# Kernel optimization log

Hardware: AMD Instinct MI355X
Metric: run time of the kernel (lower is better)

Reference implementation:

```python
import jax, jax.numpy as jnp
import numpy as np

B, H, L, D = 2, 16, 2048, 64

def setup_inputs() -> dict:
    key = jax.random.key(0)
    kq, kk, kv, km = jax.random.split(key, 4)
    q = jax.random.normal(kq, (B, H, L, D), dtype=jnp.float32)
    k = jax.random.normal(kk, (B, H, L, D), dtype=jnp.float32)
    v = jax.random.normal(kv, (B, H, L, D), dtype=jnp.float32)
    mask = jax.random.randint(km, (B, 1, L, L), 0, 2, dtype=jnp.int32)
    return {"q": q, "k": k, "v": v, "mask": mask}

def reference(q, k, v, mask):
    d_tensor = q.shape[-1]
    # score: [B,H,L,L] = q @ k^T / sqrt(d)
    score = jnp.einsum("bhqd,bhkd->bhqk", q, k) / jnp.sqrt(jnp.float32(d_tensor))
    score = jnp.where(mask == 0, jnp.float32(-jnp.inf), score)
    score = jax.nn.softmax(score, axis=-1)
    # torch.nan_to_num(nan=0.0): rows fully masked produce NaN -> 0
    score = jnp.where(jnp.isnan(score), jnp.float32(0.0), score)
    # dropout=0.0 (eval / p=0) -> identity
    out = jnp.einsum("bhqk,bhkd->bhqd", score, v)
    return (out, score)
```

## Files before the change

### kernel.cpp

```cpp
#include <hip/hip_runtime.h>
#include <math.h>

#define B_ 2
#define H_ 16
#define L_ 2048
#define D_ 64
#define NCH (L_ / 64)
#define NWG (B_ * H_ * (L_ / 64))
#define OUT_ELEMS ((size_t)B_ * H_ * L_ * D_)
#define WPR (L_ / 16)
#define C1 0.180336880f

typedef _Float16 half8 __attribute__((ext_vector_type(8)));
typedef _Float16 half4_t __attribute__((ext_vector_type(4)));
typedef float f32x4 __attribute__((ext_vector_type(4)));
typedef int i32x4 __attribute__((ext_vector_type(4)));
typedef unsigned int u32;
typedef unsigned short u16;
typedef u16 u16x4 __attribute__((ext_vector_type(4)));
typedef u32 u32x4 __attribute__((ext_vector_type(4)));
typedef u32 u32x2 __attribute__((ext_vector_type(2)));

#define SWZ(row, colh) ((colh) ^ (((row) & 7) << 3))

__global__ __launch_bounds__(256) void pack_kernel(
    const int* __restrict__ M, u16* __restrict__ pmask)
{
  const int idx = blockIdx.x * 256 + threadIdx.x;
  const int* src = M + (size_t)idx * 16;
  u32 w = 0;
#pragma unroll
  for (int j = 0; j < 4; ++j) {
    i32x4 m = ((const i32x4*)src)[j];
#pragma unroll
    for (int r = 0; r < 4; ++r)
      w |= (m[r] != 0 ? 1u : 0u) << (j * 4 + r);
  }
  pmask[idx] = (u16)w;
}

__global__ __launch_bounds__(256, 4) void lsum_kernel(
    const float* __restrict__ Q, const float* __restrict__ K,
    const u16* __restrict__ pmask, float* __restrict__ lpart)
{
  const int qt = blockIdx.x, h = blockIdx.y;
  const int b = blockIdx.z >> 2, kq = blockIdx.z & 3;
  const int bh = b * H_ + h;
  const int q0 = qt * 64, k0 = kq * 512;
  const int tid = threadIdx.x;
  const int wv = tid >> 6, lane = tid & 63;
  const int lr = lane & 15, lg = lane >> 4;
  const int qrow = q0 + wv * 16 + lr;

  __shared__ _Float16 Kbuf[2][64 * 64];

  const float* kbase = K + (size_t)bh * L_ * D_ + (size_t)k0 * D_;
  const u16* pmrow = pmask + (size_t)(b * L_ + qrow) * WPR + (k0 >> 4);

  half8 qf[2];
  {
    const float* qr = Q + (size_t)(bh * L_ + qrow) * D_;
#pragma unroll
    for (int f = 0; f < 2; ++f) {
      f32x4 x = *(const f32x4*)(qr + f * 32 + lg * 8);
      f32x4 y = *(const f32x4*)(qr + f * 32 + lg * 8 + 4);
      qf[f] = half8{(_Float16)(x[0]*C1), (_Float16)(x[1]*C1), (_Float16)(x[2]*C1), (_Float16)(x[3]*C1),
                    (_Float16)(y[0]*C1), (_Float16)(y[1]*C1), (_Float16)(y[2]*C1), (_Float16)(y[3]*C1)};
    }
  }

  const int ksr = tid >> 2, ksd = (tid & 3) * 16;
  auto loadK4 = [&](int kc, f32x4* r) {
    const float* s = kbase + (size_t)(kc + ksr) * D_ + ksd;
    r[0] = ((const f32x4*)s)[0]; r[1] = ((const f32x4*)s)[1];
    r[2] = ((const f32x4*)s)[2]; r[3] = ((const f32x4*)s)[3];
  };
  auto writeK = [&](int buf, const f32x4* r) {
    half8 lo = half8{(_Float16)r[0][0], (_Float16)r[0][1], (_Float16)r[0][2], (_Float16)r[0][3],
                     (_Float16)r[1][0], (_Float16)r[1][1], (_Float16)r[1][2], (_Float16)r[1][3]};
    half8 hi = half8{(_Float16)r[2][0], (_Float16)r[2][1], (_Float16)r[2][2], (_Float16)r[2][3],
                     (_Float16)r[3][0], (_Float16)r[3][1], (_Float16)r[3][2], (_Float16)r[3][3]};
    *(half8*)&Kbuf[buf][(ksr << 6) + SWZ(ksr, ksd)] = lo;
    *(half8*)&Kbuf[buf][(ksr << 6) + SWZ(ksr, ksd + 8)] = hi;
  };

  float l_l = 0.f;
  {
    f32x4 kr[4];
    loadK4(0, kr);
    writeK(0, kr);
  }
  __syncthreads();

  for (int c = 0; c < 8; ++c) {
    const int kc = c * 64, cur = c & 1;
    f32x4 kr[4];
    if (c < 7) loadK4(kc + 64, kr);
    u16x4 pm = *(const u16x4*)(pmrow + c * 4);

    f32x4 acc[4] = {f32x4{0,0,0,0}, f32x4{0,0,0,0}, f32x4{0,0,0,0}, f32x4{0,0,0,0}};
    __builtin_amdgcn_s_setprio(1);
#pragma unroll
    for (int kb = 0; kb < 4; ++kb) {
      int row = kb * 16 + lr;
      half8 a0 = *(const half8*)&Kbuf[cur][(row << 6) + SWZ(row, lg * 8)];
      half8 a1 = *(const half8*)&Kbuf[cur][(row << 6) + SWZ(row, 32 + lg * 8)];
      acc[kb] = __builtin_amdgcn_mfma_f32_16x16x32_f16(a0, qf[0], acc[kb], 0, 0, 0);
      acc[kb] = __builtin_amdgcn_mfma_f32_16x16x32_f16(a1, qf[1], acc[kb], 0, 0, 0);
    }
    __builtin_amdgcn_s_setprio(0);

    float cs = 0.f;
#pragma unroll
    for (int kb = 0; kb < 4; ++kb)
#pragma unroll
      for (int r = 0; r < 4; ++r)
        cs += exp2f(((pm[kb] >> (lg * 4 + r)) & 1) ? acc[kb][r] : -INFINITY);
    l_l += cs;

    if (c < 7) writeK(cur ^ 1, kr);
    __syncthreads();
  }

  l_l += __shfl_xor(l_l, 16);
  l_l += __shfl_xor(l_l, 32);
  if (lg == 0)
    lpart[((size_t)kq * 32 + bh) * L_ + qrow] = l_l;
}

__global__ __launch_bounds__(256, 4) void attn_kernel(
    const float* __restrict__ Q, const float* __restrict__ K,
    const float* __restrict__ V, const u16* __restrict__ pmask,
    const float* __restrict__ lpart,
    float* __restrict__ out, float* __restrict__ score)
{
  const int bid = blockIdx.x;
  const int lid = (bid & 7) * (NWG / 8) + (bid >> 3);
  const int qt = lid & 31, h = (lid >> 5) & 15, b = lid >> 9;

  const int bh = b * H_ + h;
  const int q0 = qt * 64;
  const int tid = threadIdx.x;
  const int wv = tid >> 6, lane = tid & 63;
  const int lr = lane & 15, lg = lane >> 4;
  const int qrow = q0 + wv * 16 + lr;

  __shared__ _Float16 Klds[2][64 * 64];
  __shared__ _Float16 Vlds[2][64 * 64];

  const float* kbase = K + (size_t)bh * L_ * D_;
  const float* vbase = V + (size_t)bh * L_ * D_;
  const u16* pmrow = pmask + (size_t)(b * L_ + qrow) * WPR;
  float* srow = score + ((size_t)bh * L_ + qrow) * L_;
  float* ob = out + (size_t)(bh * L_ + q0) * D_;

  float lsum = 0.f;
#pragma unroll
  for (int kq = 0; kq < 4; ++kq)
    lsum += lpart[((size_t)kq * 32 + bh) * L_ + qrow];
  const float inv_l = (lsum > 0.f) ? 1.f / lsum : 0.f;

  half8 qf[2];
  {
    const float* qr = Q + (size_t)(bh * L_ + qrow) * D_;
#pragma unroll
    for (int f = 0; f < 2; ++f) {
      f32x4 x = *(const f32x4*)(qr + f * 32 + lg * 8);
      f32x4 y = *(const f32x4*)(qr + f * 32 + lg * 8 + 4);
      qf[f] = half8{(_Float16)(x[0]*C1), (_Float16)(x[1]*C1), (_Float16)(x[2]*C1), (_Float16)(x[3]*C1),
                    (_Float16)(y[0]*C1), (_Float16)(y[1]*C1), (_Float16)(y[2]*C1), (_Float16)(y[3]*C1)};
    }
  }

  const int ksr = tid >> 2, ksd = (tid & 3) * 16;
  const int vk0 = (tid & 15) * 4, vd0 = (tid >> 4) * 4;

  auto loadK4 = [&](int kc, f32x4* r) {
    const float* s = kbase + (size_t)(kc + ksr) * D_ + ksd;
    r[0] = ((const f32x4*)s)[0]; r[1] = ((const f32x4*)s)[1];
    r[2] = ((const f32x4*)s)[2]; r[3] = ((const f32x4*)s)[3];
  };
  auto writeK = [&](int buf, const f32x4* r) {
    half8 lo = half8{(_Float16)r[0][0], (_Float16)r[0][1], (_Float16)r[0][2], (_Float16)r[0][3],
                     (_Float16)r[1][0], (_Float16)r[1][1], (_Float16)r[1][2], (_Float16)r[1][3]};
    half8 hi = half8{(_Float16)r[2][0], (_Float16)r[2][1], (_Float16)r[2][2], (_Float16)r[2][3],
                     (_Float16)r[3][0], (_Float16)r[3][1], (_Float16)r[3][2], (_Float16)r[3][3]};
    *(half8*)&Klds[buf][(ksr << 6) + SWZ(ksr, ksd)] = lo;
    *(half8*)&Klds[buf][(ksr << 6) + SWZ(ksr, ksd + 8)] = hi;
  };
  auto loadV4 = [&](int kc, f32x4* r) {
#pragma unroll
    for (int i = 0; i < 4; ++i)
      r[i] = *(const f32x4*)(vbase + (size_t)(kc + vk0 + i) * D_ + vd0);
  };
  auto writeV = [&](int buf, const f32x4* r) {
#pragma unroll
    for (int j = 0; j < 4; ++j) {
      int row = vd0 + j;
      *(half4_t*)&Vlds[buf][(row << 6) + SWZ(row, vk0)] =
          half4_t{(_Float16)r[0][j], (_Float16)r[1][j],
                  (_Float16)r[2][j], (_Float16)r[3][j]};
    }
  };

  {
    f32x4 kr[4], vr[4];
    loadK4(0, kr);
    loadV4(0, vr);
    writeK(0, kr);
    writeV(0, vr);
  }
  __syncthreads();

  f32x4 o_acc[4] = {f32x4{0,0,0,0}, f32x4{0,0,0,0}, f32x4{0,0,0,0}, f32x4{0,0,0,0}};

  const int s0lane = lr + 32 * (lg & 1);
  const int s1lane = s0lane + 16;
  const bool hisel = (lg & 2) != 0;

  for (int c = 0; c < NCH; ++c) {
    const int kc = c * 64, cur = c & 1;
    f32x4 krP[4], vrP[4];
    if (c < NCH - 1) {
      loadK4(kc + 64, krP);
      loadV4(kc + 64, vrP);
    }
    u16x4 pm = *(const u16x4*)(pmrow + c * 4);

    f32x4 acc[4] = {f32x4{0,0,0,0}, f32x4{0,0,0,0}, f32x4{0,0,0,0}, f32x4{0,0,0,0}};
    __builtin_amdgcn_s_setprio(1);
#pragma unroll
    for (int kb = 0; kb < 4; ++kb) {
      int row = kb * 16 + lr;
      half8 a0 = *(const half8*)&Klds[cur][(row << 6) + SWZ(row, lg * 8)];
      half8 a1 = *(const half8*)&Klds[cur][(row << 6) + SWZ(row, 32 + lg * 8)];
      acc[kb] = __builtin_amdgcn_mfma_f32_16x16x32_f16(a0, qf[0], acc[kb], 0, 0, 0);
      acc[kb] = __builtin_amdgcn_mfma_f32_16x16x32_f16(a1, qf[1], acc[kb], 0, 0, 0);
    }
    __builtin_amdgcn_s_setprio(0);

    u32 phu[8];
#pragma unroll
    for (int kb = 0; kb < 4; ++kb) {
      f32x4 p4;
#pragma unroll
      for (int r = 0; r < 4; ++r)
        p4[r] = exp2f(((pm[kb] >> (lg * 4 + r)) & 1) ? acc[kb][r] : -INFINITY) * inv_l;
      __builtin_nontemporal_store(p4, (f32x4*)(srow + kc + kb * 16 + lg * 4));
      half4_t hp = half4_t{(_Float16)p4[0], (_Float16)p4[1],
                           (_Float16)p4[2], (_Float16)p4[3]};
      u32x2 uu = __builtin_bit_cast(u32x2, hp);
      phu[2 * kb] = uu[0];
      phu[2 * kb + 1] = uu[1];
    }

    __builtin_amdgcn_s_setprio(1);
#pragma unroll
    for (int ks = 0; ks < 2; ++ks) {
      int a0 = __shfl((int)phu[4 * ks + 0], s0lane);
      int a1 = __shfl((int)phu[4 * ks + 1], s0lane);
      int a2 = __shfl((int)phu[4 * ks + 2], s0lane);
      int a3 = __shfl((int)phu[4 * ks + 3], s0lane);
      int b0 = __shfl((int)phu[4 * ks + 0], s1lane);
      int b1 = __shfl((int)phu[4 * ks + 1], s1lane);
      int b2 = __shfl((int)phu[4 * ks + 2], s1lane);
      int b3 = __shfl((int)phu[4 * ks + 3], s1lane);
      u32x4 pau = u32x4{(u32)(hisel ? a2 : a0), (u32)(hisel ? a3 : a1),
                        (u32)(hisel ? b2 : b0), (u32)(hisel ? b3 : b1)};
      half8 pa = __builtin_bit_cast(half8, pau);
#pragma unroll
      for (int db = 0; db < 4; ++db) {
        int row = db * 16 + lr;
        half8 vf = *(const half8*)&Vlds[cur][(row << 6) + SWZ(row, ks * 32 + lg * 8)];
        o_acc[db] = __builtin_amdgcn_mfma_f32_16x16x32_f16(pa, vf, o_acc[db], 0, 0, 0);
      }
    }
    __builtin_amdgcn_s_setprio(0);

    if (c < NCH - 1) {
      writeK(cur ^ 1, krP);
      writeV(cur ^ 1, vrP);
    }
    __syncthreads();
  }

#pragma unroll
  for (int db = 0; db < 4; ++db)
#pragma unroll
    for (int r = 0; r < 4; ++r)
      __builtin_nontemporal_store(
          o_acc[db][r], ob + (size_t)(wv * 16 + lg * 4 + r) * D_ + db * 16 + lr);
}

extern "C" void kernel_launch(void* const* d_in, const int* in_sizes, int n_in,
                              void* d_out, int out_size, void* d_ws, size_t ws_size,
                              hipStream_t stream) {
  const float* q = (const float*)d_in[0];
  const float* k = (const float*)d_in[1];
  const float* v = (const float*)d_in[2];
  const int* mask = (const int*)d_in[3];
  float* out = (float*)d_out;
  float* score = out + OUT_ELEMS;

  u16* pmask = (u16*)d_ws;
  float* lpart = (float*)((char*)d_ws + (1 << 20));

  pack_kernel<<<dim3(B_ * L_ * WPR / 256), 256, 0, stream>>>(mask, pmask);
  lsum_kernel<<<dim3(32, 16, 8), 256, 0, stream>>>(q, k, pmask, lpart);
  attn_kernel<<<dim3(NWG), 256, 0, stream>>>(q, k, v, pmask, lpart, out, score);
}
```

Baseline: 247.2 us.

## Split attention into split-K PV pass with atomics, separate score pass, and rescale

The row-sum pass is merged with the unnormalized P·V product, split four ways along keys, and each split adds its partial output into a zeroed buffer with atomics. A separate kernel then writes the normalized score matrix over two key halves, and a final kernel divides the output by the row sums. The aim is more workgroups and shorter serial loops than the old single 32-chunk attention kernel, and moving the large score write out of the MFMA loop. The cost is a memset, extra kernel launches, float atomics whose ordering can vary, QK^T computed twice, and P·V accumulated from unnormalized fp16 probabilities, which risks precision loss.

```diff
diff --git a/kernel.cpp b/kernel.cpp
--- a/kernel.cpp
+++ b/kernel.cpp
@@ -5,8 +5,6 @@
 #define H_ 16
 #define L_ 2048
 #define D_ 64
-#define NCH (L_ / 64)
-#define NWG (B_ * H_ * (L_ / 64))
 #define OUT_ELEMS ((size_t)B_ * H_ * L_ * D_)
 #define WPR (L_ / 16)
 #define C1 0.180336880f
@@ -39,12 +37,14 @@
   pmask[idx] = (u16)w;
 }
 
-__global__ __launch_bounds__(256, 4) void lsum_kernel(
+__global__ __launch_bounds__(256, 4) void lsum_pv_kernel(
     const float* __restrict__ Q, const float* __restrict__ K,
-    const u16* __restrict__ pmask, float* __restrict__ lpart)
+    const float* __restrict__ V, const u16* __restrict__ pmask,
+    float* __restrict__ lpart, float* __restrict__ out)
 {
-  const int qt = blockIdx.x, h = blockIdx.y;
-  const int b = blockIdx.z >> 2, kq = blockIdx.z & 3;
+  const int bid = blockIdx.x;
+  const int lid = (bid & 7) * (4096 / 8) + (bid >> 3);
+  const int qt = lid & 31, kq = (lid >> 5) & 3, h = (lid >> 7) & 15, b = lid >> 11;
   const int bh = b * H_ + h;
   const int q0 = qt * 64, k0 = kq * 512;
   const int tid = threadIdx.x;
@@ -52,113 +52,13 @@
   const int lr = lane & 15, lg = lane >> 4;
   const int qrow = q0 + wv * 16 + lr;
 
-  __shared__ _Float16 Kbuf[2][64 * 64];
-
-  const float* kbase = K + (size_t)bh * L_ * D_ + (size_t)k0 * D_;
-  const u16* pmrow = pmask + (size_t)(b * L_ + qrow) * WPR + (k0 >> 4);
-
-  half8 qf[2];
-  {
-    const float* qr = Q + (size_t)(bh * L_ + qrow) * D_;
-#pragma unroll
-    for (int f = 0; f < 2; ++f) {
-      f32x4 x = *(const f32x4*)(qr + f * 32 + lg * 8);
-      f32x4 y = *(const f32x4*)(qr + f * 32 + lg * 8 + 4);
-      qf[f] = half8{(_Float16)(x[0]*C1), (_Float16)(x[1]*C1), (_Float16)(x[2]*C1), (_Float16)(x[3]*C1),
-                    (_Float16)(y[0]*C1), (_Float16)(y[1]*C1), (_Float16)(y[2]*C1), (_Float16)(y[3]*C1)};
-    }
-  }
-
-  const int ksr = tid >> 2, ksd = (tid & 3) * 16;
-  auto loadK4 = [&](int kc, f32x4* r) {
-    const float* s = kbase + (size_t)(kc + ksr) * D_ + ksd;
-    r[0] = ((const f32x4*)s)[0]; r[1] = ((const f32x4*)s)[1];
-    r[2] = ((const f32x4*)s)[2]; r[3] = ((const f32x4*)s)[3];
-  };
-  auto writeK = [&](int buf, const f32x4* r) {
-    half8 lo = half8{(_Float16)r[0][0], (_Float16)r[0][1], (_Float16)r[0][2], (_Float16)r[0][3],
-                     (_Float16)r[1][0], (_Float16)r[1][1], (_Float16)r[1][2], (_Float16)r[1][3]};
-    half8 hi = half8{(_Float16)r[2][0], (_Float16)r[2][1], (_Float16)r[2][2], (_Float16)r[2][3],
-                     (_Float16)r[3][0], (_Float16)r[3][1], (_Float16)r[3][2], (_Float16)r[3][3]};
-    *(half8*)&Kbuf[buf][(ksr << 6) + SWZ(ksr, ksd)] = lo;
-    *(half8*)&Kbuf[buf][(ksr << 6) + SWZ(ksr, ksd + 8)] = hi;
-  };
-
-  float l_l = 0.f;
-  {
-    f32x4 kr[4];
-    loadK4(0, kr);
-    writeK(0, kr);
-  }
-  __syncthreads();
-
-  for (int c = 0; c < 8; ++c) {
-    const int kc = c * 64, cur = c & 1;
-    f32x4 kr[4];
-    if (c < 7) loadK4(kc + 64, kr);
-    u16x4 pm = *(const u16x4*)(pmrow + c * 4);
-
-    f32x4 acc[4] = {f32x4{0,0,0,0}, f32x4{0,0,0,0}, f32x4{0,0,0,0}, f32x4{0,0,0,0}};
-    __builtin_amdgcn_s_setprio(1);
-#pragma unroll
-    for (int kb = 0; kb < 4; ++kb) {
-      int row = kb * 16 + lr;
-      half8 a0 = *(const half8*)&Kbuf[cur][(row << 6) + SWZ(row, lg * 8)];
-      half8 a1 = *(const half8*)&Kbuf[cur][(row << 6) + SWZ(row, 32 + lg * 8)];
-      acc[kb] = __builtin_amdgcn_mfma_f32_16x16x32_f16(a0, qf[0], acc[kb], 0, 0, 0);
-      acc[kb] = __builtin_amdgcn_mfma_f32_16x16x32_f16(a1, qf[1], acc[kb], 0, 0, 0);
-    }
-    __builtin_amdgcn_s_setprio(0);
-
-    float cs = 0.f;
-#pragma unroll
-    for (int kb = 0; kb < 4; ++kb)
-#pragma unroll
-      for (int r = 0; r < 4; ++r)
-        cs += exp2f(((pm[kb] >> (lg * 4 + r)) & 1) ? acc[kb][r] : -INFINITY);
-    l_l += cs;
-
-    if (c < 7) writeK(cur ^ 1, kr);
-    __syncthreads();
-  }
-
-  l_l += __shfl_xor(l_l, 16);
-  l_l += __shfl_xor(l_l, 32);
-  if (lg == 0)
-    lpart[((size_t)kq * 32 + bh) * L_ + qrow] = l_l;
-}
-
-__global__ __launch_bounds__(256, 4) void attn_kernel(
-    const float* __restrict__ Q, const float* __restrict__ K,
-    const float* __restrict__ V, const u16* __restrict__ pmask,
-    const float* __restrict__ lpart,
-    float* __restrict__ out, float* __restrict__ score)
-{
-  const int bid = blockIdx.x;
-  const int lid = (bid & 7) * (NWG / 8) + (bid >> 3);
-  const int qt = lid & 31, h = (lid >> 5) & 15, b = lid >> 9;
-
-  const int bh = b * H_ + h;
-  const int q0 = qt * 64;
-  const int tid = threadIdx.x;
-  const int wv = tid >> 6, lane = tid & 63;
-  const int lr = lane & 15, lg = lane >> 4;
-  const int qrow = q0 + wv * 16 + lr;
-
   __shared__ _Float16 Klds[2][64 * 64];
   __shared__ _Float16 Vlds[2][64 * 64];
 
-  const float* kbase = K + (size_t)bh * L_ * D_;
-  const float* vbase = V + (size_t)bh * L_ * D_;
-  const u16* pmrow = pmask + (size_t)(b * L_ + qrow) * WPR;
-  float* srow = score + ((size_t)bh * L_ + qrow) * L_;
+  const float* kbase = K + ((size_t)bh * L_ + k0) * D_;
+  const float* vbase = V + ((size_t)bh * L_ + k0) * D_;
+  const u16* pmrow = pmask + (size_t)(b * L_ + qrow) * WPR + (k0 >> 4);
   float* ob = out + (size_t)(bh * L_ + q0) * D_;
-
-  float lsum = 0.f;
-#pragma unroll
-  for (int kq = 0; kq < 4; ++kq)
-    lsum += lpart[((size_t)kq * 32 + bh) * L_ + qrow];
-  const float inv_l = (lsum > 0.f) ? 1.f / lsum : 0.f;
 
   half8 qf[2];
   {
@@ -205,26 +105,22 @@
 
   {
     f32x4 kr[4], vr[4];
-    loadK4(0, kr);
-    loadV4(0, vr);
-    writeK(0, kr);
-    writeV(0, vr);
+    loadK4(0, kr); loadV4(0, vr);
+    writeK(0, kr); writeV(0, vr);
   }
   __syncthreads();
 
+  float l_l = 0.f;
   f32x4 o_acc[4] = {f32x4{0,0,0,0}, f32x4{0,0,0,0}, f32x4{0,0,0,0}, f32x4{0,0,0,0}};
 
   const int s0lane = lr + 32 * (lg & 1);
   const int s1lane = s0lane + 16;
   const bool hisel = (lg & 2) != 0;
 
-  for (int c = 0; c < NCH; ++c) {
+  for (int c = 0; c < 8; ++c) {
     const int kc = c * 64, cur = c & 1;
     f32x4 krP[4], vrP[4];
-    if (c < NCH - 1) {
-      loadK4(kc + 64, krP);
-      loadV4(kc + 64, vrP);
-    }
+    if (c < 7) { loadK4(kc + 64, krP); loadV4(kc + 64, vrP); }
     u16x4 pm = *(const u16x4*)(pmrow + c * 4);
 
     f32x4 acc[4] = {f32x4{0,0,0,0}, f32x4{0,0,0,0}, f32x4{0,0,0,0}, f32x4{0,0,0,0}};
@@ -244,9 +140,10 @@
     for (int kb = 0; kb < 4; ++kb) {
       f32x4 p4;
 #pragma unroll
-      for (int r = 0; r < 4; ++r)
-        p4[r] = exp2f(((pm[kb] >> (lg * 4 + r)) & 1) ? acc[kb][r] : -INFINITY) * inv_l;
-      __builtin_nontemporal_store(p4, (f32x4*)(srow + kc + kb * 16 + lg * 4));
+      for (int r = 0; r < 4; ++r) {
+        p4[r] = exp2f(((pm[kb] >> (lg * 4 + r)) & 1) ? acc[kb][r] : -INFINITY);
+        l_l += p4[r];
+      }
       half4_t hp = half4_t{(_Float16)p4[0], (_Float16)p4[1],
                            (_Float16)p4[2], (_Float16)p4[3]};
       u32x2 uu = __builtin_bit_cast(u32x2, hp);
@@ -277,19 +174,130 @@
     }
     __builtin_amdgcn_s_setprio(0);
 
-    if (c < NCH - 1) {
-      writeK(cur ^ 1, krP);
-      writeV(cur ^ 1, vrP);
-    }
+    if (c < 7) { writeK(cur ^ 1, krP); writeV(cur ^ 1, vrP); }
     __syncthreads();
   }
 
+  l_l += __shfl_xor(l_l, 16);
+  l_l += __shfl_xor(l_l, 32);
+  if (lg == 0)
+    lpart[((size_t)kq * 32 + bh) * L_ + qrow] = l_l;
+
 #pragma unroll
   for (int db = 0; db < 4; ++db)
 #pragma unroll
     for (int r = 0; r < 4; ++r)
-      __builtin_nontemporal_store(
-          o_acc[db][r], ob + (size_t)(wv * 16 + lg * 4 + r) * D_ + db * 16 + lr);
+      atomicAdd(&ob[(size_t)(wv * 16 + lg * 4 + r) * D_ + db * 16 + lr],
+                o_acc[db][r]);
+}
+
+__global__ __launch_bounds__(256, 8) void score_kernel(
+    const float* __restrict__ Q, const float* __restrict__ K,
+    const u16* __restrict__ pmask, const float* __restrict__ lpart,
+    float* __restrict__ score)
+{
+  const int bid = blockIdx.x;
+  const int lid = (bid & 7) * (2048 / 8) + (bid >> 3);
+  const int qt = lid & 31, kh = (lid >> 5) & 1, h = (lid >> 6) & 15, b = lid >> 10;
+  const int bh = b * H_ + h;
+  const int q0 = qt * 64, k0 = kh * 1024;
+  const int tid = threadIdx.x;
+  const int wv = tid >> 6, lane = tid & 63;
+  const int lr = lane & 15, lg = lane >> 4;
+  const int qrow = q0 + wv * 16 + lr;
+
+  __shared__ _Float16 Kbuf[2][64 * 64];
+
+  const float* kbase = K + ((size_t)bh * L_ + k0) * D_;
+  const u16* pmrow = pmask + (size_t)(b * L_ + qrow) * WPR + (k0 >> 4);
+  float* srow = score + ((size_t)bh * L_ + qrow) * L_ + k0;
+
+  float lsum = 0.f;
+#pragma unroll
+  for (int kq = 0; kq < 4; ++kq)
+    lsum += lpart[((size_t)kq * 32 + bh) * L_ + qrow];
+  const float inv_l = (lsum > 0.f) ? 1.f / lsum : 0.f;
+
+  half8 qf[2];
+  {
+    const float* qr = Q + (size_t)(bh * L_ + qrow) * D_;
+#pragma unroll
+    for (int f = 0; f < 2; ++f) {
+      f32x4 x = *(const f32x4*)(qr + f * 32 + lg * 8);
+      f32x4 y = *(const f32x4*)(qr + f * 32 + lg * 8 + 4);
+      qf[f] = half8{(_Float16)(x[0]*C1), (_Float16)(x[1]*C1), (_Float16)(x[2]*C1), (_Float16)(x[3]*C1),
+                    (_Float16)(y[0]*C1), (_Float16)(y[1]*C1), (_Float16)(y[2]*C1), (_Float16)(y[3]*C1)};
+    }
+  }
+
+  const int ksr = tid >> 2, ksd = (tid & 3) * 16;
+  auto loadK4 = [&](int kc, f32x4* r) {
+    const float* s = kbase + (size_t)(kc + ksr) * D_ + ksd;
+    r[0] = ((const f32x4*)s)[0]; r[1] = ((const f32x4*)s)[1];
+    r[2] = ((const f32x4*)s)[2]; r[3] = ((const f32x4*)s)[3];
+  };
+  auto writeK = [&](int buf, const f32x4* r) {
+    half8 lo = half8{(_Float16)r[0][0], (_Float16)r[0][1], (_Float16)r[0][2], (_Float16)r[0][3],
+                     (_Float16)r[1][0], (_Float16)r[1][1], (_Float16)r[1][2], (_Float16)r[1][3]};
+    half8 hi = half8{(_Float16)r[2][0], (_Float16)r[2][1], (_Float16)r[2][2], (_Float16)r[2][3],
+                     (_Float16)r[3][0], (_Float16)r[3][1], (_Float16)r[3][2], (_Float16)r[3][3]};
+    *(half8*)&Kbuf[buf][(ksr << 6) + SWZ(ksr, ksd)] = lo;
+    *(half8*)&Kbuf[buf][(ksr << 6) + SWZ(ksr, ksd + 8)] = hi;
+  };
+
+  {
+    f32x4 kr[4];
+    loadK4(0, kr);
+    writeK(0, kr);
+  }
+  __syncthreads();
+
+  for (int c = 0; c < 16; ++c) {
+    const int kc = c * 64, cur = c & 1;
+    f32x4 kr[4];
+    if (c < 15) loadK4(kc + 64, kr);
+    u16x4 pm = *(const u16x4*)(pmrow + c * 4);
+
+    f32x4 acc[4] = {f32x4{0,0,0,0}, f32x4{0,0,0,0}, f32x4{0,0,0,0}, f32x4{0,0,0,0}};
+    __builtin_amdgcn_s_setprio(1);
+#pragma unroll
+    for (int kb = 0; kb < 4; ++kb) {
+      int row = kb * 16 + lr;
+      half8 a0 = *(const half8*)&Kbuf[cur][(row << 6) + SWZ(row, lg * 8)];
+      half8 a1 = *(const half8*)&Kbuf[cur][(row << 6) + SWZ(row, 32 + lg * 8)];
+      acc[kb] = __builtin_amdgcn_mfma_f32_16x16x32_f16(a0, qf[0], acc[kb], 0, 0, 0);
+      acc[kb] = __builtin_amdgcn_mfma_f32_16x16x32_f16(a1, qf[1], acc[kb], 0, 0, 0);
+    }
+    __builtin_amdgcn_s_setprio(0);
+
+#pragma unroll
+    for (int kb = 0; kb < 4; ++kb) {
+      f32x4 p4;
+#pragma unroll
+      for (int r = 0; r < 4; ++r)
+        p4[r] = exp2f(((pm[kb] >> (lg * 4 + r)) & 1) ? acc[kb][r] : -INFINITY) * inv_l;
+      __builtin_nontemporal_store(p4, (f32x4*)(srow + kc + kb * 16 + lg * 4));
+    }
+
+    if (c < 15) writeK(cur ^ 1, kr);
+    __syncthreads();
+  }
+}
+
+__global__ __launch_bounds__(256) void scale_kernel(
+    const float* __restrict__ lpart, float* __restrict__ out)
+{
+  const int idx = blockIdx.x * 256 + threadIdx.x;
+  const int row = idx >> 4;
+  const int bh = row >> 11, qrow = row & (L_ - 1);
+  float ls = lpart[(size_t)(0 * 32 + bh) * L_ + qrow]
+           + lpart[(size_t)(1 * 32 + bh) * L_ + qrow]
+           + lpart[(size_t)(2 * 32 + bh) * L_ + qrow]
+           + lpart[(size_t)(3 * 32 + bh) * L_ + qrow];
+  const float inv = (ls > 0.f) ? 1.f / ls : 0.f;
+  f32x4 v = ((const f32x4*)out)[idx];
+  v[0] *= inv; v[1] *= inv; v[2] *= inv; v[3] *= inv;
+  __builtin_nontemporal_store(v, (f32x4*)out + idx);
 }
 
 extern "C" void kernel_launch(void* const* d_in, const int* in_sizes, int n_in,
@@ -305,7 +313,9 @@
   u16* pmask = (u16*)d_ws;
   float* lpart = (float*)((char*)d_ws + (1 << 20));
 
+  hipMemsetAsync(out, 0, OUT_ELEMS * sizeof(float), stream);
   pack_kernel<<<dim3(B_ * L_ * WPR / 256), 256, 0, stream>>>(mask, pmask);
-  lsum_kernel<<<dim3(32, 16, 8), 256, 0, stream>>>(q, k, pmask, lpart);
-  attn_kernel<<<dim3(NWG), 256, 0, stream>>>(q, k, v, pmask, lpart, out, score);
-}
+  lsum_pv_kernel<<<dim3(4096), 256, 0, stream>>>(q, k, v, pmask, lpart, out);
+  score_kernel<<<dim3(2048), 256, 0, stream>>>(q, k, pmask, lpart, score);
+  scale_kernel<<<dim3(OUT_ELEMS / 4 / 256), 256, 0, stream>>>(lpart, out);
+}
```

After: 345.7 us. 1.4x slower.

## Split attention key range across two workgroups and combine partial outputs

Applied to the files above, without the earlier changes.

Splits the attention kernel's key dimension in two, so each workgroup handles half of the keys. This doubles the grid from 1024 to 2048 blocks and gives the GPU more parallelism and better latency hiding. Each half writes its partial output to its own buffer, and a new combine kernel adds the halves. Because the softmax normalizer is precomputed globally, the partial sums can simply be added. This costs an extra kernel launch plus an extra write and read of the output-sized buffer, and it falls back to the full kernel if the workspace is too small.

```diff
diff --git a/kernel.cpp b/kernel.cpp
--- a/kernel.cpp
+++ b/kernel.cpp
@@ -5,8 +5,6 @@
 #define H_ 16
 #define L_ 2048
 #define D_ 64
-#define NCH (L_ / 64)
-#define NWG (B_ * H_ * (L_ / 64))
 #define OUT_ELEMS ((size_t)B_ * H_ * L_ * D_)
 #define WPR (L_ / 16)
 #define C1 0.180336880f
@@ -54,7 +52,7 @@
 
   __shared__ _Float16 Kbuf[2][64 * 64];
 
-  const float* kbase = K + (size_t)bh * L_ * D_ + (size_t)k0 * D_;
+  const float* kbase = K + ((size_t)bh * L_ + k0) * D_;
   const u16* pmrow = pmask + (size_t)(b * L_ + qrow) * WPR + (k0 >> 4);
 
   half8 qf[2];
@@ -128,16 +126,12 @@
     lpart[((size_t)kq * 32 + bh) * L_ + qrow] = l_l;
 }
 
-__global__ __launch_bounds__(256, 4) void attn_kernel(
-    const float* __restrict__ Q, const float* __restrict__ K,
-    const float* __restrict__ V, const u16* __restrict__ pmask,
-    const float* __restrict__ lpart,
-    float* __restrict__ out, float* __restrict__ score)
-{
-  const int bid = blockIdx.x;
-  const int lid = (bid & 7) * (NWG / 8) + (bid >> 3);
-  const int qt = lid & 31, h = (lid >> 5) & 15, b = lid >> 9;
-
+template <int KCH>
+__device__ __forceinline__ void attn_body(
+    const float* Q, const float* K, const float* V,
+    const u16* pmask, const float* lpart,
+    float* obase, float* score, int b, int h, int qt, int k0)
+{
   const int bh = b * H_ + h;
   const int q0 = qt * 64;
   const int tid = threadIdx.x;
@@ -148,11 +142,11 @@
   __shared__ _Float16 Klds[2][64 * 64];
   __shared__ _Float16 Vlds[2][64 * 64];
 
-  const float* kbase = K + (size_t)bh * L_ * D_;
-  const float* vbase = V + (size_t)bh * L_ * D_;
-  const u16* pmrow = pmask + (size_t)(b * L_ + qrow) * WPR;
-  float* srow = score + ((size_t)bh * L_ + qrow) * L_;
-  float* ob = out + (size_t)(bh * L_ + q0) * D_;
+  const float* kbase = K + ((size_t)bh * L_ + k0) * D_;
+  const float* vbase = V + ((size_t)bh * L_ + k0) * D_;
+  const u16* pmrow = pmask + (size_t)(b * L_ + qrow) * WPR + (k0 >> 4);
+  float* srow = score + ((size_t)bh * L_ + qrow) * L_ + k0;
+  float* ob = obase + (size_t)(bh * L_ + q0) * D_;
 
   float lsum = 0.f;
 #pragma unroll
@@ -205,10 +199,8 @@
 
   {
     f32x4 kr[4], vr[4];
-    loadK4(0, kr);
-    loadV4(0, vr);
-    writeK(0, kr);
-    writeV(0, vr);
+    loadK4(0, kr); loadV4(0, vr);
+    writeK(0, kr); writeV(0, vr);
   }
   __syncthreads();
 
@@ -218,10 +210,10 @@
   const int s1lane = s0lane + 16;
   const bool hisel = (lg & 2) != 0;
 
-  for (int c = 0; c < NCH; ++c) {
+  for (int c = 0; c < KCH; ++c) {
     const int kc = c * 64, cur = c & 1;
     f32x4 krP[4], vrP[4];
-    if (c < NCH - 1) {
+    if (c < KCH - 1) {
       loadK4(kc + 64, krP);
       loadV4(kc + 64, vrP);
     }
@@ -277,7 +269,7 @@
     }
     __builtin_amdgcn_s_setprio(0);
 
-    if (c < NCH - 1) {
+    if (c < KCH - 1) {
       writeK(cur ^ 1, krP);
       writeV(cur ^ 1, vrP);
     }
@@ -288,8 +280,42 @@
   for (int db = 0; db < 4; ++db)
 #pragma unroll
     for (int r = 0; r < 4; ++r)
-      __builtin_nontemporal_store(
-          o_acc[db][r], ob + (size_t)(wv * 16 + lg * 4 + r) * D_ + db * 16 + lr);
+      ob[(size_t)(wv * 16 + lg * 4 + r) * D_ + db * 16 + lr] = o_acc[db][r];
+}
+
+__global__ __launch_bounds__(256, 4) void attn_split_kernel(
+    const float* __restrict__ Q, const float* __restrict__ K,
+    const float* __restrict__ V, const u16* __restrict__ pmask,
+    const float* __restrict__ lpart,
+    float* __restrict__ op0, float* __restrict__ op1, float* __restrict__ score)
+{
+  const int bid = blockIdx.x;
+  const int lid = (bid & 7) * (2048 / 8) + (bid >> 3);
+  const int qt = lid & 31, kh = (lid >> 5) & 1, h = (lid >> 6) & 15, b = lid >> 10;
+  attn_body<16>(Q, K, V, pmask, lpart, kh ? op1 : op0, score,
+                b, h, qt, kh * 1024);
+}
+
+__global__ __launch_bounds__(256, 4) void attn_full_kernel(
+    const float* __restrict__ Q, const float* __restrict__ K,
+    const float* __restrict__ V, const u16* __restrict__ pmask,
+    const float* __restrict__ lpart,
+    float* __restrict__ out, float* __restrict__ score)
+{
+  const int bid = blockIdx.x;
+  const int lid = (bid & 7) * (1024 / 8) + (bid >> 3);
+  const int qt = lid & 31, h = (lid >> 5) & 15, b = lid >> 9;
+  attn_body<32>(Q, K, V, pmask, lpart, out, score, b, h, qt, 0);
+}
+
+__global__ __launch_bounds__(256) void combine_kernel(
+    const float* __restrict__ op1, float* __restrict__ out)
+{
+  const int idx = blockIdx.x * 256 + threadIdx.x;
+  f32x4 a = ((const f32x4*)out)[idx];
+  f32x4 bq = ((const f32x4*)op1)[idx];
+  a[0] += bq[0]; a[1] += bq[1]; a[2] += bq[2]; a[3] += bq[3];
+  __builtin_nontemporal_store(a, (f32x4*)out + idx);
 }
 
 extern "C" void kernel_launch(void* const* d_in, const int* in_sizes, int n_in,
@@ -304,8 +330,17 @@
 
   u16* pmask = (u16*)d_ws;
   float* lpart = (float*)((char*)d_ws + (1 << 20));
+  float* op1 = (float*)((char*)d_ws + (2 << 20));
+  const size_t need = (size_t)(2 << 20) + OUT_ELEMS * sizeof(float);
 
   pack_kernel<<<dim3(B_ * L_ * WPR / 256), 256, 0, stream>>>(mask, pmask);
   lsum_kernel<<<dim3(32, 16, 8), 256, 0, stream>>>(q, k, pmask, lpart);
-  attn_kernel<<<dim3(NWG), 256, 0, stream>>>(q, k, v, pmask, lpart, out, score);
-}
+  if (ws_size >= need) {
+    attn_split_kernel<<<dim3(2048), 256, 0, stream>>>(q, k, v, pmask, lpart,
+                                                      out, op1, score);
+    combine_kernel<<<dim3(OUT_ELEMS / 4 / 256), 256, 0, stream>>>(op1, out);
+  } else {
+    attn_full_kernel<<<dim3(1024), 256, 0, stream>>>(q, k, v, pmask, lpart,
+                                                     out, score);
+  }
+}
```

Result: no change. 244.5 us (-1.1%).
